# Kernel optimization log

Measured on AMD Instinct MI355X. Metric: run time of the kernel, lower is better.

Reference implementation:

```python
import jax, jax.numpy as jnp
import numpy as np

RANK = 16
ALPHA = 16.0
IN_F = 4096
OUT_F = 11008
TOKENS = 64


def setup_inputs() -> dict:
    key = jax.random.key(0)
    k_x, k_w, k_s, k_a, k_b, k_bias = jax.random.split(key, 6)
    return {
        "x": jax.random.normal(k_x, (TOKENS, IN_F), dtype=jnp.float32),
        "weight_int4": jax.random.normal(k_w, (OUT_F, IN_F), dtype=jnp.float32),
        "weight_scale": jax.random.uniform(k_s, (OUT_F,), dtype=jnp.float32),
        "lora_A": jax.random.normal(k_a, (RANK, IN_F), dtype=jnp.float32) * 0.01,
        "lora_B": jax.random.normal(k_b, (OUT_F, RANK), dtype=jnp.float32),
        "bias": jax.random.normal(k_bias, (OUT_F,), dtype=jnp.float32),
    }


def reference(x, weight_int4, weight_scale, lora_A, lora_B, bias):
    # Dequantize: per-output-channel scale.  [out, in]
    weight = weight_int4 * weight_scale[:, None]
    # LoRA delta: B @ A scaled by alpha/rank.  [out, in]
    lora_weight = (lora_B @ lora_A) * (ALPHA / RANK)
    effective_weight = weight + lora_weight
    # F.linear: x @ W^T + b  ->  [tokens, out]
    return x @ effective_weight.T + bias
```

## Files before the change

### kernel.cpp

```cpp
#include <hip/hip_runtime.h>
#include <hip/hip_bf16.h>
#include <cstdint>

#define TOK   64
#define INF   4096
#define OUTF  11008
#define NBLK  172
#define KCHUNKS 128

using bf16x8  = __attribute__((ext_vector_type(8))) __bf16;
using floatx4 = __attribute__((ext_vector_type(4))) float;

union B8u { uint32_t u[4]; uint4 q; bf16x8 v; };

__device__ __forceinline__ uint32_t hi2(float a, float b) {
    return (__float_as_uint(a) >> 16) | (__float_as_uint(b) & 0xffff0000u);
}
__device__ __forceinline__ float losub(float x) {
    return x - __uint_as_float(__float_as_uint(x) & 0xffff0000u);
}

__global__ __launch_bounds__(256) void k_prep_x(const float* __restrict__ x,
        unsigned short* __restrict__ xh, unsigned short* __restrict__ xl) {
    int idx  = blockIdx.x * 256 + threadIdx.x;
    int j    = idx & 7;
    int lane = (idx >> 3) & 63;
    int kc   = (idx >> 9) & 127;
    int mt   = idx >> 16;
    int row  = mt * 16 + (lane & 15);
    int col  = kc * 32 + ((lane >> 4) << 3) + j;
    float v  = x[(size_t)row * INF + col];
    uint32_t u = __float_as_uint(v);
    float lo = losub(v);
    xh[idx] = (unsigned short)(u >> 16);
    xl[idx] = (unsigned short)(__float_as_uint(lo) >> 16);
}

__global__ __launch_bounds__(256) void k_lora_t(const float* __restrict__ x,
        const float* __restrict__ A, float* __restrict__ tm) {
    __shared__ float4 xs[INF / 4];
    int t = blockIdx.x, tid = threadIdx.x;
    const float4* xr = (const float4*)(x + (size_t)t * INF);
    for (int i = tid; i < INF / 4; i += 256) xs[i] = xr[i];
    __syncthreads();
    int wv = tid >> 6, lane = tid & 63;
#pragma unroll
    for (int rr = 0; rr < 4; ++rr) {
        int r = wv * 4 + rr;
        const float4* ar = (const float4*)(A + (size_t)r * INF);
        float s = 0.f;
        for (int i = lane; i < INF / 4; i += 64) {
            float4 a = xs[i], b = ar[i];
            s += a.x * b.x + a.y * b.y + a.z * b.z + a.w * b.w;
        }
#pragma unroll
        for (int off = 32; off > 0; off >>= 1) s += __shfl_down(s, off);
        if (lane == 0) tm[t * 16 + r] = s;
    }
}

template<int QCNT, bool ATOMIC>
__global__ __launch_bounds__(256) void k_main(const float* __restrict__ W,
        const uint4* __restrict__ xh, const uint4* __restrict__ xl,
        const float* __restrict__ scale, float* __restrict__ part,
        float* __restrict__ out) {
    constexpr int KC = KCHUNKS / QCNT;
    int lane = threadIdx.x & 63;
    int wv   = threadIdx.x >> 6;
    int nb   = blockIdx.x % NBLK;
    int q    = blockIdx.x / NBLK;
    int orow = nb * 64 + wv * 16 + (lane & 15);
    int quad = lane >> 4;

    const float* wp = W + (size_t)orow * INF + q * (KC * 32) + quad * 8;
    int xoff = q * KC * 64 + lane;

    floatx4 acc[4] = {};

    constexpr int D = 4;
    float4 wA[D], wB[D];
#pragma unroll
    for (int d = 0; d < D; ++d) {
        wA[d] = *(const float4*)(wp + d * 32);
        wB[d] = *(const float4*)(wp + d * 32 + 4);
    }

#pragma unroll 1
    for (int base = 0; base < KC; base += D) {
#pragma unroll
        for (int d = 0; d < D; ++d) {
            int kc = base + d;
            int xbase = xoff + kc * 64;
            B8u ah[4], al[4];
#pragma unroll
            for (int mt = 0; mt < 4; ++mt) {
                ah[mt].q = xh[mt * 8192 + xbase];
                al[mt].q = xl[mt * 8192 + xbase];
            }
            float4 w0 = wA[d], w1 = wB[d];
            if (base + D < KC) {
                wA[d] = *(const float4*)(wp + (size_t)(base + D + d) * 32);
                wB[d] = *(const float4*)(wp + (size_t)(base + D + d) * 32 + 4);
            }
            B8u wh, wl;
            wh.u[0] = hi2(w0.x, w0.y);  wh.u[1] = hi2(w0.z, w0.w);
            wh.u[2] = hi2(w1.x, w1.y);  wh.u[3] = hi2(w1.z, w1.w);
            wl.u[0] = hi2(losub(w0.x), losub(w0.y));
            wl.u[1] = hi2(losub(w0.z), losub(w0.w));
            wl.u[2] = hi2(losub(w1.x), losub(w1.y));
            wl.u[3] = hi2(losub(w1.z), losub(w1.w));
#pragma unroll
            for (int mt = 0; mt < 4; ++mt) {
                acc[mt] = __builtin_amdgcn_mfma_f32_16x16x32_bf16(ah[mt].v, wh.v, acc[mt], 0, 0, 0);
                acc[mt] = __builtin_amdgcn_mfma_f32_16x16x32_bf16(ah[mt].v, wl.v, acc[mt], 0, 0, 0);
                acc[mt] = __builtin_amdgcn_mfma_f32_16x16x32_bf16(al[mt].v, wh.v, acc[mt], 0, 0, 0);
            }
        }
    }

#pragma unroll
    for (int mt = 0; mt < 4; ++mt) {
        int token = mt * 16 + quad * 4;
#pragma unroll
        for (int r = 0; r < 4; ++r) {
            if constexpr (ATOMIC) {
                atomicAdd(&out[(size_t)(token + r) * OUTF + orow], scale[orow] * acc[mt][r]);
            } else {
                part[((size_t)q * TOK + token + r) * OUTF + orow] = acc[mt][r];
            }
        }
    }
}

template<int QCNT>
__global__ __launch_bounds__(256) void k_post(const float* __restrict__ part,
        const float* __restrict__ scale, const float* __restrict__ bias,
        const float* __restrict__ lB, const float* __restrict__ tm,
        float* __restrict__ out) {
    int o = blockIdx.x * 256 + threadIdx.x;
    int t = blockIdx.y;
    if (o >= OUTF) return;
    float s = 0.f;
#pragma unroll
    for (int qq = 0; qq < QCNT; ++qq)
        s += part[((size_t)qq * TOK + t) * OUTF + o];
    const float4* Br = (const float4*)(lB + (size_t)o * 16);
    const float4* tr = (const float4*)(tm + (size_t)t * 16);
    float l = 0.f;
#pragma unroll
    for (int i = 0; i < 4; ++i) {
        float4 b = Br[i], tt = tr[i];
        l += b.x * tt.x + b.y * tt.y + b.z * tt.z + b.w * tt.w;
    }
    out[(size_t)t * OUTF + o] = s * scale[o] + l + bias[o];
}

__global__ __launch_bounds__(256) void k_pre(const float* __restrict__ bias,
        const float* __restrict__ lB, const float* __restrict__ tm,
        float* __restrict__ out) {
    int o = blockIdx.x * 256 + threadIdx.x;
    int t = blockIdx.y;
    if (o >= OUTF) return;
    const float4* Br = (const float4*)(lB + (size_t)o * 16);
    const float4* tr = (const float4*)(tm + (size_t)t * 16);
    float l = 0.f;
#pragma unroll
    for (int i = 0; i < 4; ++i) {
        float4 b = Br[i], tt = tr[i];
        l += b.x * tt.x + b.y * tt.y + b.z * tt.z + b.w * tt.w;
    }
    out[(size_t)t * OUTF + o] = l + bias[o];
}

extern "C" void kernel_launch(void* const* d_in, const int* in_sizes, int n_in,
                              void* d_out, int out_size, void* d_ws, size_t ws_size,
                              hipStream_t stream) {
    const float* x     = (const float*)d_in[0];
    const float* W     = (const float*)d_in[1];
    const float* scale = (const float*)d_in[2];
    const float* lA    = (const float*)d_in[3];
    const float* lB    = (const float*)d_in[4];
    const float* bias  = (const float*)d_in[5];
    float* out = (float*)d_out;

    char* ws = (char*)d_ws;
    unsigned short* xh = (unsigned short*)(ws);
    unsigned short* xl = (unsigned short*)(ws + 524288);
    float* tm   = (float*)(ws + 1048576);
    float* part = (float*)(ws + 1052672);
    const size_t base_ws = 1052672;
    const size_t need8 = base_ws + 8ull * TOK * OUTF * 4;
    const size_t need4 = base_ws + 4ull * TOK * OUTF * 4;

    k_prep_x<<<1024, 256, 0, stream>>>(x, xh, xl);
    k_lora_t<<<TOK, 256, 0, stream>>>(x, lA, tm);

    if (ws_size >= need8) {
        k_main<8, false><<<NBLK * 8, 256, 0, stream>>>(W, (const uint4*)xh,
                (const uint4*)xl, scale, part, out);
        k_post<8><<<dim3(43, TOK), 256, 0, stream>>>(part, scale, bias, lB, tm, out);
    } else if (ws_size >= need4) {
        k_main<4, false><<<NBLK * 4, 256, 0, stream>>>(W, (const uint4*)xh,
                (const uint4*)xl, scale, part, out);
        k_post<4><<<dim3(43, TOK), 256, 0, stream>>>(part, scale, bias, lB, tm, out);
    } else {
        k_pre<<<dim3(43, TOK), 256, 0, stream>>>(bias, lB, tm, out);
        k_main<8, true><<<NBLK * 8, 256, 0, stream>>>(W, (const uint4*)xh,
                (const uint4*)xl, scale, nullptr, out);
    }
}
```

Measured before the change: 334.7 us.

## Stage split activation tiles in shared memory and widen LoRA projection grid

```diff
diff --git a/kernel.cpp b/kernel.cpp
--- a/kernel.cpp
+++ b/kernel.cpp
@@ -38,70 +38,78 @@
 
 __global__ __launch_bounds__(256) void k_lora_t(const float* __restrict__ x,
         const float* __restrict__ A, float* __restrict__ tm) {
-    __shared__ float4 xs[INF / 4];
-    int t = blockIdx.x, tid = threadIdx.x;
+    int t = blockIdx.x, wv = threadIdx.x >> 6, lane = threadIdx.x & 63;
+    int r = blockIdx.y * 4 + wv;
     const float4* xr = (const float4*)(x + (size_t)t * INF);
-    for (int i = tid; i < INF / 4; i += 256) xs[i] = xr[i];
-    __syncthreads();
-    int wv = tid >> 6, lane = tid & 63;
-#pragma unroll
-    for (int rr = 0; rr < 4; ++rr) {
-        int r = wv * 4 + rr;
-        const float4* ar = (const float4*)(A + (size_t)r * INF);
-        float s = 0.f;
-        for (int i = lane; i < INF / 4; i += 64) {
-            float4 a = xs[i], b = ar[i];
-            s += a.x * b.x + a.y * b.y + a.z * b.z + a.w * b.w;
-        }
-#pragma unroll
-        for (int off = 32; off > 0; off >>= 1) s += __shfl_down(s, off);
-        if (lane == 0) tm[t * 16 + r] = s;
-    }
+    const float4* ar = (const float4*)(A + (size_t)r * INF);
+    float s = 0.f;
+#pragma unroll
+    for (int i = 0; i < INF / 4 / 64; ++i) {
+        float4 a = xr[lane + i * 64], b = ar[lane + i * 64];
+        s += a.x * b.x + a.y * b.y + a.z * b.z + a.w * b.w;
+    }
+#pragma unroll
+    for (int off = 32; off > 0; off >>= 1) s += __shfl_down(s, off);
+    if (lane == 0) tm[t * 16 + r] = s;
 }
 
 template<int QCNT, bool ATOMIC>
-__global__ __launch_bounds__(256) void k_main(const float* __restrict__ W,
+__global__ __launch_bounds__(256, 2) void k_main(const float* __restrict__ W,
         const uint4* __restrict__ xh, const uint4* __restrict__ xl,
         const float* __restrict__ scale, float* __restrict__ part,
         float* __restrict__ out) {
-    constexpr int KC = KCHUNKS / QCNT;
-    int lane = threadIdx.x & 63;
-    int wv   = threadIdx.x >> 6;
+    constexpr int KC  = KCHUNKS / QCNT;
+    constexpr int SKC = 8;
+    constexpr int NST = KC / SKC;
+    static_assert(KC % SKC == 0, "");
+    __shared__ uint4 xs[2][4][SKC][64];
+
+    int tid  = threadIdx.x;
+    int lane = tid & 63;
+    int wv   = tid >> 6;
     int nb   = blockIdx.x % NBLK;
     int q    = blockIdx.x / NBLK;
     int orow = nb * 64 + wv * 16 + (lane & 15);
     int quad = lane >> 4;
 
-    const float* wp = W + (size_t)orow * INF + q * (KC * 32) + quad * 8;
-    int xoff = q * KC * 64 + lane;
+    const float* wp = W + (size_t)orow * INF + (size_t)q * (KC * 32) + quad * 8;
 
     floatx4 acc[4] = {};
 
-    constexpr int D = 4;
-    float4 wA[D], wB[D];
-#pragma unroll
-    for (int d = 0; d < D; ++d) {
-        wA[d] = *(const float4*)(wp + d * 32);
-        wB[d] = *(const float4*)(wp + d * 32 + 4);
-    }
-
-#pragma unroll 1
-    for (int base = 0; base < KC; base += D) {
-#pragma unroll
-        for (int d = 0; d < D; ++d) {
-            int kc = base + d;
-            int xbase = xoff + kc * 64;
-            B8u ah[4], al[4];
-#pragma unroll
-            for (int mt = 0; mt < 4; ++mt) {
-                ah[mt].q = xh[mt * 8192 + xbase];
-                al[mt].q = xl[mt * 8192 + xbase];
-            }
+    for (int st = 0; st < NST; ++st) {
+        int kc0 = st * SKC;
+        if (st > 0) __syncthreads();
+
+        constexpr int CPT = (2 * 4 * SKC * 64) / 256;
+        uint4 tmp[CPT];
+#pragma unroll
+        for (int it = 0; it < CPT; ++it) {
+            int idx = tid + it * 256;
+            int l2 = idx & 63, kc = (idx >> 6) & (SKC - 1);
+            int mt = (idx >> 9) & 3, hl = idx >> 11;
+            const uint4* src = hl ? xl : xh;
+            tmp[it] = src[((size_t)mt * KCHUNKS + q * KC + kc0 + kc) * 64 + l2];
+        }
+#pragma unroll
+        for (int it = 0; it < CPT; ++it) {
+            int idx = tid + it * 256;
+            int l2 = idx & 63, kc = (idx >> 6) & (SKC - 1);
+            int mt = (idx >> 9) & 3, hl = idx >> 11;
+            xs[hl][mt][kc][l2] = tmp[it];
+        }
+
+        float4 wA[SKC], wB[SKC];
+#pragma unroll
+        for (int d = 0; d < SKC; ++d) {
+            wA[d] = *(const float4*)(wp + (size_t)(kc0 + d) * 32);
+            wB[d] = *(const float4*)(wp + (size_t)(kc0 + d) * 32 + 4);
+        }
+
+        __syncthreads();
+
+#pragma unroll
+        for (int d = 0; d < SKC; ++d) {
             float4 w0 = wA[d], w1 = wB[d];
-            if (base + D < KC) {
-                wA[d] = *(const float4*)(wp + (size_t)(base + D + d) * 32);
-                wB[d] = *(const float4*)(wp + (size_t)(base + D + d) * 32 + 4);
-            }
             B8u wh, wl;
             wh.u[0] = hi2(w0.x, w0.y);  wh.u[1] = hi2(w0.z, w0.w);
             wh.u[2] = hi2(w1.x, w1.y);  wh.u[3] = hi2(w1.z, w1.w);
@@ -111,9 +119,12 @@
             wl.u[3] = hi2(losub(w1.z), losub(w1.w));
 #pragma unroll
             for (int mt = 0; mt < 4; ++mt) {
-                acc[mt] = __builtin_amdgcn_mfma_f32_16x16x32_bf16(ah[mt].v, wh.v, acc[mt], 0, 0, 0);
-                acc[mt] = __builtin_amdgcn_mfma_f32_16x16x32_bf16(ah[mt].v, wl.v, acc[mt], 0, 0, 0);
-                acc[mt] = __builtin_amdgcn_mfma_f32_16x16x32_bf16(al[mt].v, wh.v, acc[mt], 0, 0, 0);
+                B8u ah, al;
+                ah.q = xs[0][mt][d][lane];
+                al.q = xs[1][mt][d][lane];
+                acc[mt] = __builtin_amdgcn_mfma_f32_16x16x32_bf16(ah.v, wh.v, acc[mt], 0, 0, 0);
+                acc[mt] = __builtin_amdgcn_mfma_f32_16x16x32_bf16(ah.v, wl.v, acc[mt], 0, 0, 0);
+                acc[mt] = __builtin_amdgcn_mfma_f32_16x16x32_bf16(al.v, wh.v, acc[mt], 0, 0, 0);
             }
         }
     }
@@ -193,7 +204,7 @@
     const size_t need4 = base_ws + 4ull * TOK * OUTF * 4;
 
     k_prep_x<<<1024, 256, 0, stream>>>(x, xh, xl);
-    k_lora_t<<<TOK, 256, 0, stream>>>(x, lA, tm);
+    k_lora_t<<<dim3(TOK, 4), 256, 0, stream>>>(x, lA, tm);
 
     if (ws_size >= need8) {
         k_main<8, false><<<NBLK * 8, 256, 0, stream>>>(W, (const uint4*)xh,
```

Result: faster. 276.0 us (-17.5%).
